# Optimization experiments

Measured on AMD Instinct MI355X. Metric: run time of the kernel, lower is better.

## Reference

```python
import jax, jax.numpy as jnp
import numpy as np

DIM = 1024
HEADS = 16

def setup_inputs() -> dict:
    key = jax.random.key(0)
    ks = jax.random.split(key, 9)
    s = DIM ** -0.5  # init scale for weights
    x = jax.random.normal(ks[0], (2, 2048, DIM), dtype=jnp.float32)
    wq = jax.random.normal(ks[1], (DIM, DIM), dtype=jnp.float32) * s
    bq = jax.random.normal(ks[2], (DIM,), dtype=jnp.float32) * 0.01
    wk = jax.random.normal(ks[3], (DIM, DIM), dtype=jnp.float32) * s
    bk = jax.random.normal(ks[4], (DIM,), dtype=jnp.float32) * 0.01
    wv = jax.random.normal(ks[5], (DIM, DIM), dtype=jnp.float32) * s
    bv = jax.random.normal(ks[6], (DIM,), dtype=jnp.float32) * 0.01
    wo = jax.random.normal(ks[7], (DIM, DIM), dtype=jnp.float32) * s
    bo = jax.random.normal(ks[8], (DIM,), dtype=jnp.float32) * 0.01
    return {"x": x, "wq": wq, "bq": bq, "wk": wk, "bk": bk,
            "wv": wv, "bv": bv, "wo": wo, "bo": bo}

def reference(x, wq, bq, wk, bk, wv, bv, wo, bo):
    b, l, dim = x.shape
    h = HEADS
    d = dim // h
    scale = dim ** -0.5  # NOTE: full dim, as in the original module
    # torch Linear: x @ W.T + b
    def proj(w, bias):
        y = jnp.einsum('bld,ed->ble', x, w) + bias
        return y.reshape(b, l, h, d).transpose(0, 2, 1, 3)  # b h l d
    q = proj(wq, bq)
    k = proj(wk, bk)
    v = proj(wv, bv)
    attn = jnp.einsum('bhid,bhjd->bhij', q, k) * scale
    attn = jax.nn.softmax(attn, axis=-1)
    out = jnp.einsum('bhij,bhjd->bhid', attn, v)
    out = out.transpose(0, 2, 1, 3).reshape(b, l, dim)
    return jnp.einsum('ble,fe->blf', out, wo) + bo
```

## Files before the change

kernel.cpp:

```cpp
#include <hip/hip_runtime.h>
#include <hip/hip_bf16.h>
#include <stdint.h>


typedef __attribute__((ext_vector_type(8))) short short8;
typedef __attribute__((ext_vector_type(4))) float f32x4;
typedef __attribute__((ext_vector_type(16))) float f32x16;

#define MFMA(a, b, c) __builtin_amdgcn_mfma_f32_16x16x32_bf16((a), (b), (c), 0, 0, 0)
#define MFMA32(a, b, c) __builtin_amdgcn_mfma_f32_32x32x16_bf16((a), (b), (c), 0, 0, 0)

#if __has_builtin(__builtin_amdgcn_exp2f)
#define EXP2(x) __builtin_amdgcn_exp2f(x)
#else
#define EXP2(x) exp2f(x)
#endif

__device__ __forceinline__ ushort f2bf(float f) {
  uint32_t u = __builtin_bit_cast(uint32_t, f);
  u += 0x7fffu + ((u >> 16) & 1u);
  return (ushort)(u >> 16);
}

__device__ __forceinline__ uint32_t pkbf(float lo, float hi) {
  __hip_bfloat162 h = __float22bfloat162_rn(make_float2(lo, hi));
  uint32_t u;
  __builtin_memcpy(&u, &h, 4);
  return u;
}

__device__ __forceinline__ uint32_t cvtpk(float lo, float hi) {
  uint32_t u;
  asm("v_cvt_pk_bf16_f32 %0, %1, %2" : "=v"(u) : "v"(lo), "v"(hi));
  return u;
}

__device__ __forceinline__ void pl32swap(uint32_t& a, uint32_t& b) {
  asm("v_permlane32_swap_b32 %0, %1" : "+v"(a), "+v"(b));
}

__device__ __forceinline__ void gl_lds16(const void* g, void* l) {
  __builtin_amdgcn_global_load_lds(
      (const __attribute__((address_space(1))) unsigned int*)g,
      (__attribute__((address_space(3))) unsigned int*)l, 16, 0, 0);
}

__global__ __launch_bounds__(256) void convert_all(
    const float* __restrict__ x, const float* __restrict__ wq,
    const float* __restrict__ wk, const float* __restrict__ wv,
    const float* __restrict__ wo, ushort* __restrict__ dst) {
  size_t i4 = (size_t)blockIdx.x * 256 + threadIdx.x;
  size_t e = i4 * 4;
  const float* src; size_t off;
  if (e < 4194304u)      { src = x;  off = e; }
  else if (e < 5242880u) { src = wq; off = e - 4194304u; }
  else if (e < 6291456u) { src = wk; off = e - 5242880u; }
  else if (e < 7340032u) { src = wv; off = e - 6291456u; }
  else                   { src = wo; off = e - 7340032u; }
  float4 v = *(const float4*)(src + off);
  ushort4 o = { f2bf(v.x), f2bf(v.y), f2bf(v.z), f2bf(v.w) };
  *(ushort4*)(dst + e) = o;
}

__global__ __launch_bounds__(256) void gemm_qkv(
    const ushort* __restrict__ xb,
    const ushort* __restrict__ wqb, const ushort* __restrict__ wkb,
    const ushort* __restrict__ wvb,
    const float* __restrict__ bq_, const float* __restrict__ bk_,
    const float* __restrict__ bv_,
    ushort* __restrict__ qout, ushort* __restrict__ kout,
    ushort* __restrict__ vtout) {
  __shared__ __align__(16) ushort As[128 * 32];
  __shared__ __align__(16) ushort Bs[128 * 32];
  const int z = blockIdx.z;
  const int bn = blockIdx.x, bm = blockIdx.y;
  const int t = threadIdx.x;
  const int w = t >> 6, lane = t & 63;
  const int wr = w >> 1, wc = w & 1;
  const int l15 = lane & 15, l4 = lane >> 4;

  const ushort* wb = (z == 0) ? wqb : (z == 1 ? wkb : wvb);
  const float* bias = (z == 0) ? bq_ : (z == 1 ? bk_ : bv_);

  f32x4 acc[4][4] = {};

  for (int kt = 0; kt < 32; ++kt) {
    __syncthreads();
#pragma unroll
    for (int rr = 0; rr < 2; ++rr) {
      int c = t + rr * 256;
      int row = c >> 2, cin = c & 3;
      gl_lds16(xb + (bm * 128 + row) * 1024 + kt * 32 + cin * 8, (void*)&As[c * 8]);
      gl_lds16(wb + (bn * 128 + row) * 1024 + kt * 32 + cin * 8, (void*)&Bs[c * 8]);
    }
    __syncthreads();
    short8 af[4], bfr[4];
#pragma unroll
    for (int mf = 0; mf < 4; ++mf)
      af[mf] = *(const short8*)&As[(wr * 64 + mf * 16 + l15) * 32 + l4 * 8];
#pragma unroll
    for (int nf = 0; nf < 4; ++nf)
      bfr[nf] = *(const short8*)&Bs[(wc * 64 + nf * 16 + l15) * 32 + l4 * 8];
    __builtin_amdgcn_s_setprio(1);
#pragma unroll
    for (int mf = 0; mf < 4; ++mf)
#pragma unroll
      for (int nf = 0; nf < 4; ++nf)
        acc[mf][nf] = MFMA(af[mf], bfr[nf], acc[mf][nf]);
    __builtin_amdgcn_s_setprio(0);
  }

  const float qsc = 0.045084439f;
#pragma unroll
  for (int mf = 0; mf < 4; ++mf) {
#pragma unroll
    for (int nf = 0; nf < 4; ++nf) {
      int n = bn * 128 + wc * 64 + nf * 16 + l15;
      int m0 = bm * 128 + wr * 64 + mf * 16 + l4 * 4;
      float b = bias[n];
      float vals[4];
#pragma unroll
      for (int r = 0; r < 4; ++r) vals[r] = acc[mf][nf][r] + b;
      int bb = m0 >> 11, l0 = m0 & 2047;
      int h = n >> 6, d = n & 63;
      int bh = bb * 16 + h;
      if (z == 2) {
        *(uint2*)&vtout[(bh * 64 + d) * 2048 + l0] =
            make_uint2(pkbf(vals[0], vals[1]), pkbf(vals[2], vals[3]));
      } else if (z == 0) {
#pragma unroll
        for (int r = 0; r < 4; ++r)
          qout[(bh * 2048 + l0 + r) * 64 + d] = f2bf(vals[r] * qsc);
      } else {
#pragma unroll
        for (int r = 0; r < 4; ++r)
          kout[(bh * 2048 + l0 + r) * 64 + d] = f2bf(vals[r]);
      }
    }
  }
}

__global__ __launch_bounds__(256, 2) void attn(
    const ushort* __restrict__ qb, const ushort* __restrict__ kb,
    const ushort* __restrict__ vtb, ushort* __restrict__ aout) {
  __shared__ __align__(16) ushort Ks[4][64 * 64];
  __shared__ __align__(16) ushort Vs[4][64 * 64];
  const int bid = blockIdx.x;
  const int xcd = bid & 7, idx = bid >> 3;
  const int bh = xcd * 4 + (idx >> 4);
  const int it = idx & 15;
  const int t = threadIdx.x, w = t >> 6, lane = t & 63;
  const int l31 = lane & 31, hi = lane >> 5;
  const size_t kvbase = (size_t)bh * (2048 * 64);
  const int i0 = it * 128 + w * 32;

  const int c0 = t, c1 = t + 256;
  const int r0 = c0 >> 3, s0 = (c0 & 7) ^ (r0 & 7);
  const int r1 = c1 >> 3, s1 = (c1 & 7) ^ (r1 & 7);

#define STAGE(bufi, jts)                                                     \
  {                                                                          \
    const int j0s = (jts) * 64;                                              \
    gl_lds16(kb + kvbase + (size_t)(j0s + r0) * 64 + s0 * 8,                 \
             (void*)&Ks[bufi][c0 * 8]);                                      \
    gl_lds16(kb + kvbase + (size_t)(j0s + r1) * 64 + s1 * 8,                 \
             (void*)&Ks[bufi][c1 * 8]);                                      \
    gl_lds16(vtb + kvbase + (size_t)r0 * 2048 + j0s + s0 * 8,                \
             (void*)&Vs[bufi][c0 * 8]);                                      \
    gl_lds16(vtb + kvbase + (size_t)r1 * 2048 + j0s + s1 * 8,                \
             (void*)&Vs[bufi][c1 * 8]);                                      \
  }

  short8 qf[4];
#pragma unroll
  for (int ks = 0; ks < 4; ++ks)
    qf[ks] = *(const short8*)&qb[kvbase + (size_t)(i0 + l31) * 64 + ks * 16 + hi * 8];

  f32x16 ot0 = {}, ot1 = {};
  float ts0 = 0.f, ts1 = 0.f, ts2 = 0.f, ts3 = 0.f;

  STAGE(0, 0);
  STAGE(1, 1);

  for (int jt = 0; jt < 32; ++jt) {
    const int cur = jt & 3;
    const int nxt = (jt + 2) & 3;
    const int jts = (jt + 2 < 32) ? (jt + 2) : 31;
    STAGE(nxt, jts);
    asm volatile("s_waitcnt vmcnt(8)" ::: "memory");
    __builtin_amdgcn_s_barrier();
    asm volatile("" ::: "memory");

    const ushort* Kc = &Ks[cur][0];
    const ushort* Vc = &Vs[cur][0];

    const int swz = (l31 & 7);
    short8 ka0[4], ka1[4], va0[4], va1[4];
#pragma unroll
    for (int ks = 0; ks < 4; ++ks) {
      int ck = (ks * 2 + hi) ^ swz;
      ka0[ks] = *(const short8*)&Kc[l31 * 64 + ck * 8];
      ka1[ks] = *(const short8*)&Kc[(32 + l31) * 64 + ck * 8];
    }
#pragma unroll
    for (int b = 0; b < 4; ++b) {
      int cv = (b * 2 + hi) ^ swz;
      va0[b] = *(const short8*)&Vc[l31 * 64 + cv * 8];
      va1[b] = *(const short8*)&Vc[(32 + l31) * 64 + cv * 8];
    }

    f32x16 st0 = {}, st1 = {};
    __builtin_amdgcn_s_setprio(1);
#pragma unroll
    for (int ks = 0; ks < 4; ++ks) {
      st0 = MFMA32(ka0[ks], qf[ks], st0);
      st1 = MFMA32(ka1[ks], qf[ks], st1);
    }
    __builtin_amdgcn_s_setprio(0);

    f32x16 p0, p1;
#pragma unroll
    for (int r = 0; r < 16; r += 4) {
      p0[r] = EXP2(st0[r]);         ts0 += p0[r];
      p0[r + 1] = EXP2(st0[r + 1]); ts1 += p0[r + 1];
      p0[r + 2] = EXP2(st0[r + 2]); ts2 += p0[r + 2];
      p0[r + 3] = EXP2(st0[r + 3]); ts3 += p0[r + 3];
    }
#pragma unroll
    for (int r = 0; r < 16; r += 4) {
      p1[r] = EXP2(st1[r]);         ts0 += p1[r];
      p1[r + 1] = EXP2(st1[r + 1]); ts1 += p1[r + 1];
      p1[r + 2] = EXP2(st1[r + 2]); ts2 += p1[r + 2];
      p1[r + 3] = EXP2(st1[r + 3]); ts3 += p1[r + 3];
    }

    short8 pb[4];
#pragma unroll
    for (int b = 0; b < 4; ++b) {
      f32x16 pv = (b < 2) ? p0 : p1;
      const int R = 8 * (b & 1);
      uint32_t c01 = cvtpk(pv[R + 0], pv[R + 1]);
      uint32_t c23 = cvtpk(pv[R + 2], pv[R + 3]);
      uint32_t c45 = cvtpk(pv[R + 4], pv[R + 5]);
      uint32_t c67 = cvtpk(pv[R + 6], pv[R + 7]);
      pl32swap(c01, c45);
      pl32swap(c23, c67);
      union { uint32_t u[4]; short8 s; } pk;
      pk.u[0] = c01; pk.u[1] = c23; pk.u[2] = c45; pk.u[3] = c67;
      pb[b] = pk.s;
    }

    __builtin_amdgcn_s_setprio(1);
#pragma unroll
    for (int b = 0; b < 4; ++b) {
      ot0 = MFMA32(va0[b], pb[b], ot0);
      ot1 = MFMA32(va1[b], pb[b], ot1);
    }
    __builtin_amdgcn_s_setprio(0);
  }

  float lsum = (ts0 + ts1) + (ts2 + ts3);
  {
    uint32_t a = __builtin_bit_cast(uint32_t, lsum);
    uint32_t b = a;
    pl32swap(a, b);
    lsum = __builtin_bit_cast(float, a) + __builtin_bit_cast(float, b);
  }
  const int bb = bh >> 4, h = bh & 15;
  float inv = 1.0f / lsum;
  ushort* orow = aout + (size_t)(bb * 2048 + i0 + l31) * 1024 + h * 64;
#pragma unroll
  for (int mf = 0; mf < 2; ++mf) {
    f32x16 o = mf ? ot1 : ot0;
#pragma unroll
    for (int g = 0; g < 4; ++g) {
      int d0 = mf * 32 + g * 8 + hi * 4;
      *(uint2*)(orow + d0) = make_uint2(
          cvtpk(o[g * 4 + 0] * inv, o[g * 4 + 1] * inv),
          cvtpk(o[g * 4 + 2] * inv, o[g * 4 + 3] * inv));
    }
  }
#undef STAGE
}

__global__ __launch_bounds__(256) void gemm_out(
    const ushort* __restrict__ ab, const ushort* __restrict__ wob,
    const float* __restrict__ bo_, float* __restrict__ out) {
  __shared__ __align__(16) ushort As[128 * 32];
  __shared__ __align__(16) ushort Bs[128 * 32];
  const int bn = blockIdx.x, bm = blockIdx.y;
  const int t = threadIdx.x;
  const int w = t >> 6, lane = t & 63;
  const int wr = w >> 1, wc = w & 1;
  const int l15 = lane & 15, l4 = lane >> 4;

  f32x4 acc[4][4] = {};

  for (int kt = 0; kt < 32; ++kt) {
    __syncthreads();
#pragma unroll
    for (int rr = 0; rr < 2; ++rr) {
      int c = t + rr * 256;
      int row = c >> 2, cin = c & 3;
      gl_lds16(ab + (bm * 128 + row) * 1024 + kt * 32 + cin * 8, (void*)&As[c * 8]);
      gl_lds16(wob + (bn * 128 + row) * 1024 + kt * 32 + cin * 8, (void*)&Bs[c * 8]);
    }
    __syncthreads();
    short8 af[4], bfr[4];
#pragma unroll
    for (int mf = 0; mf < 4; ++mf)
      af[mf] = *(const short8*)&As[(wr * 64 + mf * 16 + l15) * 32 + l4 * 8];
#pragma unroll
    for (int nf = 0; nf < 4; ++nf)
      bfr[nf] = *(const short8*)&Bs[(wc * 64 + nf * 16 + l15) * 32 + l4 * 8];
    __builtin_amdgcn_s_setprio(1);
#pragma unroll
    for (int mf = 0; mf < 4; ++mf)
#pragma unroll
      for (int nf = 0; nf < 4; ++nf)
        acc[mf][nf] = MFMA(af[mf], bfr[nf], acc[mf][nf]);
    __builtin_amdgcn_s_setprio(0);
  }

#pragma unroll
  for (int mf = 0; mf < 4; ++mf)
#pragma unroll
    for (int nf = 0; nf < 4; ++nf) {
      int n = bn * 128 + wc * 64 + nf * 16 + l15;
      int m0 = bm * 128 + wr * 64 + mf * 16 + l4 * 4;
      float b = bo_[n];
#pragma unroll
      for (int r = 0; r < 4; ++r)
        out[(size_t)(m0 + r) * 1024 + n] = acc[mf][nf][r] + b;
    }
}

extern "C" void kernel_launch(void* const* d_in, const int* in_sizes, int n_in,
                              void* d_out, int out_size, void* d_ws, size_t ws_size,
                              hipStream_t stream) {
  const float* x  = (const float*)d_in[0];
  const float* wq = (const float*)d_in[1];
  const float* bq = (const float*)d_in[2];
  const float* wk = (const float*)d_in[3];
  const float* bk = (const float*)d_in[4];
  const float* wv = (const float*)d_in[5];
  const float* bv = (const float*)d_in[6];
  const float* wo = (const float*)d_in[7];
  const float* bo = (const float*)d_in[8];

  ushort* ws  = (ushort*)d_ws;
  ushort* xb  = ws;
  ushort* wqb = ws + 4194304;
  ushort* wkb = ws + 5242880;
  ushort* wvb = ws + 6291456;
  ushort* wob = ws + 7340032;
  ushort* qbp = ws + 8388608;
  ushort* kbp = ws + 12582912;
  ushort* vtb = ws + 16777216;
  ushort* ab  = ws + 20971520;

  convert_all<<<8192, 256, 0, stream>>>(x, wq, wk, wv, wo, ws);
  gemm_qkv<<<dim3(8, 32, 3), 256, 0, stream>>>(xb, wqb, wkb, wvb, bq, bk, bv,
                                               qbp, kbp, vtb);
  attn<<<512, 256, 0, stream>>>(qbp, kbp, vtb, ab);
  gemm_out<<<dim3(8, 32), 256, 0, stream>>>(ab, wob, bo, (float*)d_out);
}
```

Measured before the change: 113.5 us.

## Software-pipeline QK^T MFMA one tile ahead of softmax and PV

Restructures the attention inner loop so the QK^T MFMAs for the next KV tile are issued at the end of the current iteration, after the PV MFMAs and the barrier. The intent is to overlap the next tile's score computation with the exp/convert work and to shorten the dependency chain at the top of each iteration. Barrier placement and the vmcnt waits move to match. The risk is that keeping st0/st1 live across iterations raises register pressure, and the LDS buffer reuse timing changes.

```diff
diff --git a/kernel.cpp b/kernel.cpp
--- a/kernel.cpp
+++ b/kernel.cpp
@@ -171,6 +171,21 @@
              (void*)&Vs[bufi][c1 * 8]);                                      \
   }
 
+#define QKSTEP(kbuf)                                                         \
+  {                                                                          \
+    const ushort* Kc = &Ks[kbuf][0];                                         \
+    __builtin_amdgcn_s_setprio(1);                                           \
+    _Pragma("unroll")                                                        \
+    for (int ks = 0; ks < 4; ++ks) {                                         \
+      int ck = (ks * 2 + hi) ^ swz;                                          \
+      short8 a0 = *(const short8*)&Kc[l31 * 64 + ck * 8];                    \
+      short8 a1 = *(const short8*)&Kc[(32 + l31) * 64 + ck * 8];             \
+      st0 = MFMA32(a0, qf[ks], st0);                                         \
+      st1 = MFMA32(a1, qf[ks], st1);                                         \
+    }                                                                        \
+    __builtin_amdgcn_s_setprio(0);                                           \
+  }
+
   short8 qf[4];
 #pragma unroll
   for (int ks = 0; ks < 4; ++ks)
@@ -178,45 +193,29 @@
 
   f32x16 ot0 = {}, ot1 = {};
   float ts0 = 0.f, ts1 = 0.f, ts2 = 0.f, ts3 = 0.f;
+  const int swz = (l31 & 7);
 
   STAGE(0, 0);
   STAGE(1, 1);
+  asm volatile("s_waitcnt vmcnt(4)" ::: "memory");
+  __builtin_amdgcn_s_barrier();
+  asm volatile("" ::: "memory");
+
+  f32x16 st0 = {}, st1 = {};
+  QKSTEP(0);
 
   for (int jt = 0; jt < 32; ++jt) {
     const int cur = jt & 3;
-    const int nxt = (jt + 2) & 3;
-    const int jts = (jt + 2 < 32) ? (jt + 2) : 31;
-    STAGE(nxt, jts);
-    asm volatile("s_waitcnt vmcnt(8)" ::: "memory");
-    __builtin_amdgcn_s_barrier();
-    asm volatile("" ::: "memory");
-
-    const ushort* Kc = &Ks[cur][0];
+    STAGE((jt + 2) & 3, (jt + 2 < 32) ? (jt + 2) : 31);
+
     const ushort* Vc = &Vs[cur][0];
-
-    const int swz = (l31 & 7);
-    short8 ka0[4], ka1[4], va0[4], va1[4];
-#pragma unroll
-    for (int ks = 0; ks < 4; ++ks) {
-      int ck = (ks * 2 + hi) ^ swz;
-      ka0[ks] = *(const short8*)&Kc[l31 * 64 + ck * 8];
-      ka1[ks] = *(const short8*)&Kc[(32 + l31) * 64 + ck * 8];
-    }
+    short8 va0[4], va1[4];
 #pragma unroll
     for (int b = 0; b < 4; ++b) {
       int cv = (b * 2 + hi) ^ swz;
       va0[b] = *(const short8*)&Vc[l31 * 64 + cv * 8];
       va1[b] = *(const short8*)&Vc[(32 + l31) * 64 + cv * 8];
     }
-
-    f32x16 st0 = {}, st1 = {};
-    __builtin_amdgcn_s_setprio(1);
-#pragma unroll
-    for (int ks = 0; ks < 4; ++ks) {
-      st0 = MFMA32(ka0[ks], qf[ks], st0);
-      st1 = MFMA32(ka1[ks], qf[ks], st1);
-    }
-    __builtin_amdgcn_s_setprio(0);
 
     f32x16 p0, p1;
 #pragma unroll
@@ -257,6 +256,16 @@
       ot1 = MFMA32(va1[b], pb[b], ot1);
     }
     __builtin_amdgcn_s_setprio(0);
+
+    asm volatile("s_waitcnt vmcnt(4)" ::: "memory");
+    __builtin_amdgcn_s_barrier();
+    asm volatile("" ::: "memory");
+
+    if (jt < 31) {
+#pragma unroll
+      for (int r = 0; r < 16; ++r) { st0[r] = 0.f; st1[r] = 0.f; }
+      QKSTEP((jt + 1) & 3);
+    }
   }
 
   float lsum = (ts0 + ts1) + (ts2 + ts3);
@@ -281,6 +290,7 @@
     }
   }
 #undef STAGE
+#undef QKSTEP
 }
 
 __global__ __launch_bounds__(256) void gemm_out(
```

Result: no change. 112.6 us (median of 2 runs) (-0.8%).
